# Performance work log

Measured on AMD Instinct MI355X. Metric: run time of the kernel, lower is better.

## Reference

```python
import jax, jax.numpy as jnp
import numpy as np

D_MODEL, N_HEADS, D_K, BASE, EPS = 1024, 16, 64, 10000, 1e-6
SCALE = 1.0 / np.sqrt(D_K)


def rope(x):
    # x: [b, s, h, d]
    b, s, h, d = x.shape
    d2 = d // 2
    theta = 1.0 / (BASE ** (jnp.arange(0, d, 2, dtype=jnp.float32) / d))  # [d2]
    idx_theta = jnp.arange(s, dtype=jnp.float32)[:, None] * theta[None, :]  # [s, d2]
    idx_theta2 = jnp.concatenate([idx_theta, idx_theta], axis=1)  # [s, d]
    cos = jnp.cos(idx_theta2)[None, :, None, :]
    sin = jnp.sin(idx_theta2)[None, :, None, :]
    neg_half = jnp.concatenate([-x[..., d2:], x[..., :d2]], axis=-1)
    return x * cos + neg_half * sin


def setup_inputs() -> dict:
    key = jax.random.key(0)
    ks = jax.random.split(key, 10)
    B, S = 2, 2048
    std = 1.0 / np.sqrt(D_MODEL)
    return {
        "h": jax.random.normal(ks[0], (B, S, D_MODEL), dtype=jnp.float32),
        "wq": jax.random.normal(ks[1], (D_MODEL, N_HEADS * D_K), dtype=jnp.float32) * std,
        "bq": jnp.zeros((N_HEADS * D_K,), dtype=jnp.float32),
        "wk": jax.random.normal(ks[2], (D_MODEL, N_HEADS * D_K), dtype=jnp.float32) * std,
        "bk": jnp.zeros((N_HEADS * D_K,), dtype=jnp.float32),
        "wv": jax.random.normal(ks[3], (D_MODEL, N_HEADS * D_K), dtype=jnp.float32) * std,
        "bv": jnp.zeros((N_HEADS * D_K,), dtype=jnp.float32),
        "wo": jax.random.normal(ks[4], (N_HEADS * D_K, D_MODEL), dtype=jnp.float32) * std,
        "bo": jnp.zeros((D_MODEL,), dtype=jnp.float32),
        "g": jnp.ones((D_MODEL,), dtype=jnp.float32),
    }


def reference(h, wq, bq, wk, bk, wv, bv, wo, bo, g):
    B, S, _ = h.shape
    h_res = h
    # RMSNorm
    hn = h * jax.lax.rsqrt(jnp.mean(h * h, axis=-1, keepdims=True) + EPS) * g
    mh = (B, S, N_HEADS, D_K)
    q = (hn @ wq + bq).reshape(mh)
    k = (hn @ wk + bk).reshape(mh)
    v = (hn @ wv + bv).reshape(mh)
    q, k = rope(q), rope(k)
    attn = jnp.einsum('bihd,bjhd->bhij', q, k) * SCALE
    mask = jnp.tril(jnp.ones((S, S), dtype=bool))
    attn = jnp.where(mask, attn, -jnp.inf)
    attn = jax.nn.softmax(attn, axis=-1)
    out = jnp.einsum('bhij,bjhd->bihd', attn, v).reshape(B, S, N_HEADS * D_K)
    return out @ wo + bo + h_res
```

## Files before the change

### kernel.cpp

```cpp
#include <hip/hip_runtime.h>
#include <hip/hip_bf16.h>

#define D_MODEL 1024
#define NH 16
#define DK 64
#define SEQ 2048
#define BATCH 2
#define NTOK (BATCH * SEQ)
#define EPS 1e-6f

typedef __attribute__((ext_vector_type(4))) float f32x4;
typedef __attribute__((ext_vector_type(16))) float f32x16;
typedef __attribute__((ext_vector_type(8))) short s16x8;
typedef unsigned int u32;
typedef __hip_bfloat16 bf16;

#define AS1 __attribute__((address_space(1)))
#define AS3 __attribute__((address_space(3)))

static __device__ __forceinline__ s16x8 ld8(const bf16* p) {
    return *reinterpret_cast<const s16x8*>(p);
}
static __device__ __forceinline__ float b2f(short s) {
    return __uint_as_float(((u32)(unsigned short)s) << 16);
}

static __device__ __forceinline__ u32 cvtpk(float lo, float hi) {
    u32 r;
    asm volatile("v_cvt_pk_bf16_f32 %0, %1, %2" : "=v"(r) : "v"(lo), "v"(hi));
    return r;
}
static __device__ __forceinline__ void swap32(u32& a, u32& b) {
    asm volatile("v_permlane32_swap_b32 %0, %1" : "+v"(a), "+v"(b));
}
static __device__ __forceinline__ float exp2f_fast(float x) {
    float r;
    asm("v_exp_f32 %0, %1" : "=v"(r) : "v"(x));
    return r;
}
static __device__ __forceinline__ void gld_lds16(const bf16* g, bf16* l) {
    __builtin_amdgcn_global_load_lds((const AS1 void*)g, (AS3 void*)l, 16, 0, 0);
}

union W4 { s16x8 v; u32 w[4]; };

#define LDSW(arr, row, kc) ld8(&arr[(row)][(((kc) ^ ((row) & 7)) << 3)])

__global__ __launch_bounds__(256) void k_prep(const float* __restrict__ h,
                                              const float* __restrict__ g,
                                              const float* __restrict__ wq,
                                              const float* __restrict__ wk,
                                              const float* __restrict__ wv,
                                              const float* __restrict__ wo,
                                              bf16* __restrict__ hn,
                                              bf16* __restrict__ wallT,
                                              float2* __restrict__ tab) {
    const int bid = blockIdx.x;
    const int tid = threadIdx.x;
    if (bid < 4096) {
        const int row = bid;
        const float4 x = reinterpret_cast<const float4*>(h + (size_t)row * D_MODEL)[tid];
        float ss = x.x * x.x + x.y * x.y + x.z * x.z + x.w * x.w;
#pragma unroll
        for (int off = 32; off; off >>= 1) ss += __shfl_xor(ss, off);
        __shared__ float red[4];
        if ((tid & 63) == 0) red[tid >> 6] = ss;
        __syncthreads();
        const float tot = red[0] + red[1] + red[2] + red[3];
        const float rs = rsqrtf(tot * (1.0f / D_MODEL) + EPS);
        const float4 gg = reinterpret_cast<const float4*>(g)[tid];
        bf16* o = hn + (size_t)row * D_MODEL + tid * 4;
        o[0] = __float2bfloat16(x.x * rs * gg.x);
        o[1] = __float2bfloat16(x.y * rs * gg.y);
        o[2] = __float2bfloat16(x.z * rs * gg.z);
        o[3] = __float2bfloat16(x.w * rs * gg.w);
        if (row < 256) {
            const int idx = row * 256 + tid;
            const int s = idx >> 5, i = idx & 31;
            const float theta = __expf(-(float)i * 0.28782313662425572f);
            float sn, cs;
            sincosf((float)s * theta, &sn, &cs);
            tab[idx] = make_float2(cs, sn);
        }
    } else {
        __shared__ float t[32][33];
        const int bid2 = bid - 4096;
        const int kt = (bid2 & 31) * 32;
        const int by = bid2 >> 5;
        const int nt = by * 32;
        const float* W = (by < 32) ? wq : (by < 64) ? wk : (by < 96) ? wv : wo;
        const int nl = nt & (D_MODEL - 1);
        const int tx = tid & 31, ty = tid >> 5;
#pragma unroll
        for (int i = 0; i < 4; i++)
            t[ty + 8 * i][tx] = W[(size_t)(kt + ty + 8 * i) * D_MODEL + nl + tx];
        __syncthreads();
#pragma unroll
        for (int i = 0; i < 4; i++)
            wallT[(size_t)(nt + ty + 8 * i) * D_MODEL + kt + tx] = __float2bfloat16(t[tx][ty + 8 * i]);
    }
}

__global__ __launch_bounds__(256) void k_gemm64_qkv(const bf16* __restrict__ A,
                                                    const bf16* __restrict__ Bt,
                                                    const float* __restrict__ bq,
                                                    const float* __restrict__ bk,
                                                    const float* __restrict__ bv,
                                                    const float2* __restrict__ tab,
                                                    bf16* __restrict__ qb,
                                                    bf16* __restrict__ kpk,
                                                    bf16* __restrict__ vpk) {
    __shared__ __align__(16) char smem[32768];
    const int tid = threadIdx.x;
    const int w = tid >> 6, lane = tid & 63, l16 = lane & 15, lq = lane >> 4;
    const int wr = w >> 1, wc = w & 1;
    const int col0 = blockIdx.x * 64;
    const int row0 = blockIdx.y * 64;
    const int grow = lane >> 3;
    const int scol = (((lane & 7) ^ grow) << 3);

    auto stage = [&](int buf, int t) {
        bf16* as = (bf16*)(smem + buf * 16384);
        bf16* bs = (bf16*)(smem + buf * 16384 + 8192);
        const int k0 = t << 6;
        gld_lds16(A + (size_t)(row0 + w * 16 + grow) * D_MODEL + k0 + scol,      as + (w * 16) * 64);
        gld_lds16(A + (size_t)(row0 + w * 16 + 8 + grow) * D_MODEL + k0 + scol,  as + (w * 16 + 8) * 64);
        gld_lds16(Bt + (size_t)(col0 + w * 16 + grow) * D_MODEL + k0 + scol,     bs + (w * 16) * 64);
        gld_lds16(Bt + (size_t)(col0 + w * 16 + 8 + grow) * D_MODEL + k0 + scol, bs + (w * 16 + 8) * 64);
    };

    f32x4 acc[2][2];
#pragma unroll
    for (int i = 0; i < 2; i++)
#pragma unroll
        for (int j = 0; j < 2; j++) acc[i][j] = f32x4{0, 0, 0, 0};

    stage(0, 0);
    __syncthreads();
    int buf = 0;
    for (int t = 0; t < 16; t++) {
        if (t < 15) stage(buf ^ 1, t + 1);
        bf16(*As)[64] = (bf16(*)[64])(smem + buf * 16384);
        bf16(*Bs)[64] = (bf16(*)[64])(smem + buf * 16384 + 8192);
        s16x8 af[2][2], bfr[2][2];
#pragma unroll
        for (int mi = 0; mi < 2; mi++)
#pragma unroll
            for (int ks = 0; ks < 2; ks++)
                af[mi][ks] = LDSW(As, wr * 32 + mi * 16 + l16, ks * 4 + lq);
#pragma unroll
        for (int ni = 0; ni < 2; ni++)
#pragma unroll
            for (int ks = 0; ks < 2; ks++)
                bfr[ni][ks] = LDSW(Bs, wc * 32 + ni * 16 + l16, ks * 4 + lq);
        __builtin_amdgcn_s_setprio(1);
#pragma unroll
        for (int ks = 0; ks < 2; ks++)
#pragma unroll
            for (int mi = 0; mi < 2; mi++)
#pragma unroll
                for (int ni = 0; ni < 2; ni++)
                    acc[mi][ni] = __builtin_amdgcn_mfma_f32_16x16x32_bf16(af[mi][ks], bfr[ni][ks], acc[mi][ni], 0, 0, 0);
        __builtin_amdgcn_s_setprio(0);
        __syncthreads();
        buf ^= 1;
    }

    const int sect = col0 >> 10;
    const int b_ = row0 >> 11;
    const int head = (col0 & 1023) >> 6;
    if (sect == 2) {
        const int e0 = (lq & 1) * 4;
        const int tileL = (row0 & (SEQ - 1)) >> 6;
        bf16* dstH = vpk + ((size_t)(b_ * NH + head) << 17);
#pragma unroll
        for (int ni = 0; ni < 2; ni++) {
            const int dloc = wc * 32 + ni * 16 + l16;
            const float bs = bv[(col0 & 1023) + dloc];
#pragma unroll
            for (int mi = 0; mi < 2; mi++) {
                const int m = wr * 2 + mi;
                size_t off = ((((size_t)(tileL * 2 + (dloc >> 5)) * 4 + m) * 64
                               + ((lq >> 1) & 1) * 32 + (dloc & 31)) << 3) + e0;
                uint2 pv;
                pv.x = cvtpk(acc[mi][ni][0] + bs, acc[mi][ni][1] + bs);
                pv.y = cvtpk(acc[mi][ni][2] + bs, acc[mi][ni][3] + bs);
                *reinterpret_cast<uint2*>(dstH + off) = pv;
            }
        }
        return;
    }
    bf16(*Cs)[72] = (bf16(*)[72])smem;
    const float* bias = (sect == 0) ? bq : bk;
#pragma unroll
    for (int ni = 0; ni < 2; ni++) {
        const int cl = wc * 32 + ni * 16 + l16;
        const float bs = bias[(col0 & 1023) + cl];
#pragma unroll
        for (int mi = 0; mi < 2; mi++) {
            const int rl = wr * 32 + mi * 16 + lq * 4;
#pragma unroll
            for (int r = 0; r < 4; r++)
                Cs[rl + r][cl] = __float2bfloat16(acc[mi][ni][r] + bs);
        }
    }
    __syncthreads();
    const int row = tid >> 2, q = tid & 3;
    const int s_ = (row0 + row) & (SEQ - 1);
    const float2* tb = tab + s_ * 32 + q * 8;
    const float qs = (sect == 0) ? 0.18033688011112042f : 1.0f;
    const s16x8 vlo = ld8(&Cs[row][q * 8]);
    const s16x8 vhi = ld8(&Cs[row][q * 8 + 32]);
    u32 plo[4], phi[4];
#pragma unroll
    for (int e2 = 0; e2 < 4; e2++) {
        float a[2], b[2];
#pragma unroll
        for (int k = 0; k < 2; k++) {
            const int e = e2 * 2 + k;
            const float2 cs = tb[e];
            const float x1 = b2f(vlo[e]), x2 = b2f(vhi[e]);
            a[k] = (x1 * cs.x - x2 * cs.y) * qs;
            b[k] = (x2 * cs.x + x1 * cs.y) * qs;
        }
        plo[e2] = cvtpk(a[0], a[1]);
        phi[e2] = cvtpk(b[0], b[1]);
    }
    if (sect == 0) {
        bf16* qdst = qb + (((size_t)(b_ * NH + head) * SEQ + s_) << 6);
        *reinterpret_cast<uint4*>(qdst + q * 8)      = make_uint4(plo[0], plo[1], plo[2], plo[3]);
        *reinterpret_cast<uint4*>(qdst + 32 + q * 8) = make_uint4(phi[0], phi[1], phi[2], phi[3]);
    } else {
        bf16* kdst = kpk + ((size_t)(b_ * NH + head) << 17);
        const int jb = s_ >> 5, j31 = s_ & 31;
        const size_t offL = (((size_t)(jb * 4 + (q >> 1)) * 64 + (q & 1) * 32 + j31) << 3);
        const size_t offH = (((size_t)(jb * 4 + ((q + 4) >> 1)) * 64 + ((q + 4) & 1) * 32 + j31) << 3);
        *reinterpret_cast<uint4*>(kdst + offL) = make_uint4(plo[0], plo[1], plo[2], plo[3]);
        *reinterpret_cast<uint4*>(kdst + offH) = make_uint4(phi[0], phi[1], phi[2], phi[3]);
    }
}

__global__ __launch_bounds__(256) void k_attn9(const bf16* __restrict__ qg,
                                               const bf16* __restrict__ kp,
                                               const bf16* __restrict__ vp,
                                               bf16* __restrict__ ao) {
    const int tid = threadIdx.x;
    const int w = tid >> 6;
    const int lane = tid & 63;
    const int l31 = lane & 31;
    const int hi = lane >> 5;
    const int bid = blockIdx.x;
    const int blk = (bid >> 3) & 15;
    const int bh  = (bid & 7) + ((bid >> 7) << 3);
    int pos;
    switch (w) {
        case 0:  pos = blk;      break;
        case 1:  pos = 31 - blk; break;
        case 2:  pos = 32 + blk; break;
        default: pos = 63 - blk; break;
    }
    const int qw = pos << 5;
    const int qrow = qw + l31;

    const bf16* qptr = qg + (((size_t)bh * SEQ + qrow) << 6) + 8 * hi;
    s16x8 qf[4];
#pragma unroll
    for (int t = 0; t < 4; t++) qf[t] = ld8(qptr + 16 * t);

    f32x16 o0, o1;
#pragma unroll
    for (int r = 0; r < 16; r++) { o0[r] = 0.0f; o1[r] = 0.0f; }
    float l4[4] = {0.0f, 0.0f, 0.0f, 0.0f};

    const int nfull = qw >> 6;
    const int ntot  = (qw + 95) >> 6;
    const bf16* kbase = kp + ((size_t)bh << 17);
    const bf16* vbase = vp + ((size_t)bh << 17);

    s16x8 kA[8], kB[8], vC[8];
#pragma unroll
    for (int t = 0; t < 8; t++) kA[t] = ld8(kbase + (((size_t)t * 64 + lane) << 3));

    auto att_step = [&](s16x8(&KC)[8], s16x8(&KN)[8], const int kt) {
        const int kb = kt << 6;
#pragma unroll
        for (int t = 0; t < 8; t++)
            vC[t] = ld8(vbase + (((size_t)(kt * 8 + t) * 64 + lane) << 3));
        f32x16 s0, s1;
#pragma unroll
        for (int r = 0; r < 16; r++) { s0[r] = 0.0f; s1[r] = 0.0f; }
        __builtin_amdgcn_s_setprio(1);
#pragma unroll
        for (int t = 0; t < 4; t++) {
            s0 = __builtin_amdgcn_mfma_f32_32x32x16_bf16(KC[t],     qf[t], s0, 0, 0, 0);
            s1 = __builtin_amdgcn_mfma_f32_32x32x16_bf16(KC[4 + t], qf[t], s1, 0, 0, 0);
        }
        __builtin_amdgcn_s_setprio(0);
        const int ktn = (kt + 1 < ntot) ? kt + 1 : kt;
#pragma unroll
        for (int t = 0; t < 8; t++)
            KN[t] = ld8(kbase + (((size_t)(ktn * 8 + t) * 64 + lane) << 3));
        float p[32];
#pragma unroll
        for (int r = 0; r < 16; r++) { p[r] = s0[r]; p[16 + r] = s1[r]; }
        if (kt >= nfull) {
#pragma unroll
            for (int r = 0; r < 32; r++) {
                const int j = kb + 8 * (r >> 2) + (r & 3) + 4 * hi;
                if (j > qrow) p[r] = -3.0e38f;
            }
        }
#pragma unroll
        for (int r = 0; r < 32; r++) { p[r] = exp2f_fast(p[r]); l4[r & 3] += p[r]; }
        u32 pk_[16];
#pragma unroll
        for (int a = 0; a < 8; a++) {
            pk_[2 * a]     = cvtpk(p[4 * a],     p[4 * a + 1]);
            pk_[2 * a + 1] = cvtpk(p[4 * a + 2], p[4 * a + 3]);
        }
        __builtin_amdgcn_s_setprio(1);
#pragma unroll
        for (int m = 0; m < 4; m++) {
            u32 b0 = pk_[4 * m],     b2 = pk_[4 * m + 2];
            u32 b1 = pk_[4 * m + 1], b3 = pk_[4 * m + 3];
            swap32(b0, b2);
            swap32(b1, b3);
            W4 B; B.w[0] = b0; B.w[1] = b1; B.w[2] = b2; B.w[3] = b3;
            o0 = __builtin_amdgcn_mfma_f32_32x32x16_bf16(vC[m],     B.v, o0, 0, 0, 0);
            o1 = __builtin_amdgcn_mfma_f32_32x32x16_bf16(vC[4 + m], B.v, o1, 0, 0, 0);
        }
        __builtin_amdgcn_s_setprio(0);
    };

    int kt = 0;
    for (;;) {
        att_step(kA, kB, kt); if (++kt == ntot) break;
        att_step(kB, kA, kt); if (++kt == ntot) break;
    }

    float rs = (l4[0] + l4[1]) + (l4[2] + l4[3]);
    rs += __shfl_xor(rs, 32);
    const float inv = 1.0f / rs;
    const int b_ = bh >> 4, h_ = bh & (NH - 1);
    bf16* orow = ao + (((size_t)(b_ * SEQ + qrow)) << 10) + (h_ << 6);
#pragma unroll
    for (int g = 0; g < 4; g++) {
        {
            uint2 val;
            val.x = cvtpk(o0[4 * g] * inv, o0[4 * g + 1] * inv);
            val.y = cvtpk(o0[4 * g + 2] * inv, o0[4 * g + 3] * inv);
            *reinterpret_cast<uint2*>(orow + 8 * g + 4 * hi) = val;
        }
        {
            uint2 val;
            val.x = cvtpk(o1[4 * g] * inv, o1[4 * g + 1] * inv);
            val.y = cvtpk(o1[4 * g + 2] * inv, o1[4 * g + 3] * inv);
            *reinterpret_cast<uint2*>(orow + 32 + 8 * g + 4 * hi) = val;
        }
    }
}

__global__ __launch_bounds__(256) void k_gemm64_out(const bf16* __restrict__ A,
                                                    const bf16* __restrict__ Bt,
                                                    const float* __restrict__ bo,
                                                    const float* __restrict__ hres,
                                                    float* __restrict__ out) {
    __shared__ __align__(16) char smem[32768];
    const int tid = threadIdx.x;
    const int w = tid >> 6, lane = tid & 63, l16 = lane & 15, lq = lane >> 4;
    const int wr = w >> 1, wc = w & 1;
    const int col0 = blockIdx.x * 64;
    const int row0 = blockIdx.y * 64;
    const int grow = lane >> 3;
    const int scol = (((lane & 7) ^ grow) << 3);

    auto stage = [&](int buf, int t) {
        bf16* as = (bf16*)(smem + buf * 16384);
        bf16* bs = (bf16*)(smem + buf * 16384 + 8192);
        const int k0 = t << 6;
        gld_lds16(A + (size_t)(row0 + w * 16 + grow) * D_MODEL + k0 + scol,      as + (w * 16) * 64);
        gld_lds16(A + (size_t)(row0 + w * 16 + 8 + grow) * D_MODEL + k0 + scol,  as + (w * 16 + 8) * 64);
        gld_lds16(Bt + (size_t)(col0 + w * 16 + grow) * D_MODEL + k0 + scol,     bs + (w * 16) * 64);
        gld_lds16(Bt + (size_t)(col0 + w * 16 + 8 + grow) * D_MODEL + k0 + scol, bs + (w * 16 + 8) * 64);
    };

    f32x4 acc[2][2];
#pragma unroll
    for (int i = 0; i < 2; i++)
#pragma unroll
        for (int j = 0; j < 2; j++) acc[i][j] = f32x4{0, 0, 0, 0};

    stage(0, 0);
    __syncthreads();
    int buf = 0;
    for (int t = 0; t < 16; t++) {
        if (t < 15) stage(buf ^ 1, t + 1);
        bf16(*As)[64] = (bf16(*)[64])(smem + buf * 16384);
        bf16(*Bs)[64] = (bf16(*)[64])(smem + buf * 16384 + 8192);
        s16x8 af[2][2], bfr[2][2];
#pragma unroll
        for (int mi = 0; mi < 2; mi++)
#pragma unroll
            for (int ks = 0; ks < 2; ks++)
                af[mi][ks] = LDSW(As, wr * 32 + mi * 16 + l16, ks * 4 + lq);
#pragma unroll
        for (int ni = 0; ni < 2; ni++)
#pragma unroll
            for (int ks = 0; ks < 2; ks++)
                bfr[ni][ks] = LDSW(Bs, wc * 32 + ni * 16 + l16, ks * 4 + lq);
        __builtin_amdgcn_s_setprio(1);
#pragma unroll
        for (int ks = 0; ks < 2; ks++)
#pragma unroll
            for (int mi = 0; mi < 2; mi++)
#pragma unroll
                for (int ni = 0; ni < 2; ni++)
                    acc[mi][ni] = __builtin_amdgcn_mfma_f32_16x16x32_bf16(af[mi][ks], bfr[ni][ks], acc[mi][ni], 0, 0, 0);
        __builtin_amdgcn_s_setprio(0);
        __syncthreads();
        buf ^= 1;
    }
#pragma unroll
    for (int ni = 0; ni < 2; ni++) {
        const int col = col0 + wc * 32 + ni * 16 + l16;
        const float bs = bo[col];
#pragma unroll
        for (int mi = 0; mi < 2; mi++) {
#pragma unroll
            for (int r = 0; r < 4; r++) {
                const int row = row0 + wr * 32 + mi * 16 + lq * 4 + r;
                out[(size_t)row * D_MODEL + col] =
                    acc[mi][ni][r] + bs + hres[(size_t)row * D_MODEL + col];
            }
        }
    }
}

extern "C" void kernel_launch(void* const* d_in, const int* in_sizes, int n_in,
                              void* d_out, int out_size, void* d_ws, size_t ws_size,
                              hipStream_t stream) {
    (void)in_sizes; (void)n_in; (void)out_size; (void)ws_size;
    const float* h  = (const float*)d_in[0];
    const float* wq = (const float*)d_in[1];
    const float* bq = (const float*)d_in[2];
    const float* wk = (const float*)d_in[3];
    const float* bk = (const float*)d_in[4];
    const float* wv = (const float*)d_in[5];
    const float* bv = (const float*)d_in[6];
    const float* wo = (const float*)d_in[7];
    const float* bo = (const float*)d_in[8];
    const float* g  = (const float*)d_in[9];
    float* out = (float*)d_out;

    char* ws = (char*)d_ws;
    size_t off = 0;
    auto carve = [&](size_t bytes) {
        void* p = ws + off;
        off += (bytes + 255) & ~(size_t)255;
        return p;
    };
    bf16* hn    = (bf16*)carve((size_t)NTOK * D_MODEL * 2);
    bf16* wallT = (bf16*)carve((size_t)4 * D_MODEL * D_MODEL * 2);
    bf16* wqkvT = wallT;
    bf16* woT   = wallT + (size_t)3 * D_MODEL * D_MODEL;
    bf16* qb    = (bf16*)carve((size_t)BATCH * NH * SEQ * DK * 2);
    bf16* kpk   = (bf16*)carve((size_t)BATCH * NH * SEQ * DK * 2);
    bf16* vpk   = (bf16*)carve((size_t)BATCH * NH * SEQ * DK * 2);
    bf16* ao    = (bf16*)carve((size_t)NTOK * D_MODEL * 2);
    float2* tab = (float2*)carve((size_t)SEQ * 32 * sizeof(float2));

    k_prep<<<8192, 256, 0, stream>>>(h, g, wq, wk, wv, wo, hn, wallT, tab);
    k_gemm64_qkv<<<dim3(48, 64), 256, 0, stream>>>(hn, wqkvT, bq, bk, bv, tab, qb, kpk, vpk);
    k_attn9<<<512, 256, 0, stream>>>(qb, kpk, vpk, ao);
    k_gemm64_out<<<dim3(16, 64), 256, 0, stream>>>(ao, woT, bo, h, out);
}
```

Before: 107.4 us.

## Enlarge QKV and output GEMM tiles to 128x128 with K-step 32

Measured after the change: 120.0 us. +11.7%, slower.

```diff
diff --git a/kernel.cpp b/kernel.cpp
--- a/kernel.cpp
+++ b/kernel.cpp
@@ -44,7 +44,7 @@
 
 union W4 { s16x8 v; u32 w[4]; };
 
-#define LDSW(arr, row, kc) ld8(&arr[(row)][(((kc) ^ ((row) & 7)) << 3)])
+#define SW32C(row, kc) ((((kc) ^ (((row) >> 1) & 3))) << 3)
 
 __global__ __launch_bounds__(256) void k_prep(const float* __restrict__ h,
                                               const float* __restrict__ g,
@@ -101,66 +101,64 @@
     }
 }
 
-__global__ __launch_bounds__(256) void k_gemm64_qkv(const bf16* __restrict__ A,
-                                                    const bf16* __restrict__ Bt,
-                                                    const float* __restrict__ bq,
-                                                    const float* __restrict__ bk,
-                                                    const float* __restrict__ bv,
-                                                    const float2* __restrict__ tab,
-                                                    bf16* __restrict__ qb,
-                                                    bf16* __restrict__ kpk,
-                                                    bf16* __restrict__ vpk) {
+__global__ __launch_bounds__(256) void k_gemm128_qkv(const bf16* __restrict__ A,
+                                                     const bf16* __restrict__ Bt,
+                                                     const float* __restrict__ bq,
+                                                     const float* __restrict__ bk,
+                                                     const float* __restrict__ bv,
+                                                     const float2* __restrict__ tab,
+                                                     bf16* __restrict__ qb,
+                                                     bf16* __restrict__ kpk,
+                                                     bf16* __restrict__ vpk) {
     __shared__ __align__(16) char smem[32768];
     const int tid = threadIdx.x;
     const int w = tid >> 6, lane = tid & 63, l16 = lane & 15, lq = lane >> 4;
     const int wr = w >> 1, wc = w & 1;
-    const int col0 = blockIdx.x * 64;
-    const int row0 = blockIdx.y * 64;
-    const int grow = lane >> 3;
-    const int scol = (((lane & 7) ^ grow) << 3);
+    const int col0 = blockIdx.x * 128;
+    const int row0 = blockIdx.y * 128;
+    const int grow = lane >> 2;
+    const int scol = SW32C(grow, lane & 3);
 
     auto stage = [&](int buf, int t) {
         bf16* as = (bf16*)(smem + buf * 16384);
         bf16* bs = (bf16*)(smem + buf * 16384 + 8192);
-        const int k0 = t << 6;
-        gld_lds16(A + (size_t)(row0 + w * 16 + grow) * D_MODEL + k0 + scol,      as + (w * 16) * 64);
-        gld_lds16(A + (size_t)(row0 + w * 16 + 8 + grow) * D_MODEL + k0 + scol,  as + (w * 16 + 8) * 64);
-        gld_lds16(Bt + (size_t)(col0 + w * 16 + grow) * D_MODEL + k0 + scol,     bs + (w * 16) * 64);
-        gld_lds16(Bt + (size_t)(col0 + w * 16 + 8 + grow) * D_MODEL + k0 + scol, bs + (w * 16 + 8) * 64);
+        const int k0 = t << 5;
+        gld_lds16(A + (size_t)(row0 + w * 16 + grow) * D_MODEL + k0 + scol,       as + (w * 16) * 32);
+        gld_lds16(A + (size_t)(row0 + 64 + w * 16 + grow) * D_MODEL + k0 + scol,  as + (64 + w * 16) * 32);
+        gld_lds16(Bt + (size_t)(col0 + w * 16 + grow) * D_MODEL + k0 + scol,      bs + (w * 16) * 32);
+        gld_lds16(Bt + (size_t)(col0 + 64 + w * 16 + grow) * D_MODEL + k0 + scol, bs + (64 + w * 16) * 32);
     };
 
-    f32x4 acc[2][2];
-#pragma unroll
-    for (int i = 0; i < 2; i++)
-#pragma unroll
-        for (int j = 0; j < 2; j++) acc[i][j] = f32x4{0, 0, 0, 0};
+    f32x4 acc[4][4];
+#pragma unroll
+    for (int i = 0; i < 4; i++)
+#pragma unroll
+        for (int j = 0; j < 4; j++) acc[i][j] = f32x4{0, 0, 0, 0};
 
     stage(0, 0);
     __syncthreads();
     int buf = 0;
-    for (int t = 0; t < 16; t++) {
-        if (t < 15) stage(buf ^ 1, t + 1);
-        bf16(*As)[64] = (bf16(*)[64])(smem + buf * 16384);
-        bf16(*Bs)[64] = (bf16(*)[64])(smem + buf * 16384 + 8192);
-        s16x8 af[2][2], bfr[2][2];
-#pragma unroll
-        for (int mi = 0; mi < 2; mi++)
-#pragma unroll
-            for (int ks = 0; ks < 2; ks++)
-                af[mi][ks] = LDSW(As, wr * 32 + mi * 16 + l16, ks * 4 + lq);
-#pragma unroll
-        for (int ni = 0; ni < 2; ni++)
-#pragma unroll
-            for (int ks = 0; ks < 2; ks++)
-                bfr[ni][ks] = LDSW(Bs, wc * 32 + ni * 16 + l16, ks * 4 + lq);
+    for (int t = 0; t < 32; t++) {
+        if (t < 31) stage(buf ^ 1, t + 1);
+        bf16(*As)[32] = (bf16(*)[32])(smem + buf * 16384);
+        bf16(*Bs)[32] = (bf16(*)[32])(smem + buf * 16384 + 8192);
+        s16x8 af[4], bfr[4];
+#pragma unroll
+        for (int mi = 0; mi < 4; mi++) {
+            const int rr = wr * 64 + mi * 16 + l16;
+            af[mi] = ld8(&As[rr][SW32C(rr, lq)]);
+        }
+#pragma unroll
+        for (int ni = 0; ni < 4; ni++) {
+            const int rr = wc * 64 + ni * 16 + l16;
+            bfr[ni] = ld8(&Bs[rr][SW32C(rr, lq)]);
+        }
         __builtin_amdgcn_s_setprio(1);
 #pragma unroll
-        for (int ks = 0; ks < 2; ks++)
-#pragma unroll
-            for (int mi = 0; mi < 2; mi++)
-#pragma unroll
-                for (int ni = 0; ni < 2; ni++)
-                    acc[mi][ni] = __builtin_amdgcn_mfma_f32_16x16x32_bf16(af[mi][ks], bfr[ni][ks], acc[mi][ni], 0, 0, 0);
+        for (int mi = 0; mi < 4; mi++)
+#pragma unroll
+            for (int ni = 0; ni < 4; ni++)
+                acc[mi][ni] = __builtin_amdgcn_mfma_f32_16x16x32_bf16(af[mi], bfr[ni], acc[mi][ni], 0, 0, 0);
         __builtin_amdgcn_s_setprio(0);
         __syncthreads();
         buf ^= 1;
@@ -168,20 +166,19 @@
 
     const int sect = col0 >> 10;
     const int b_ = row0 >> 11;
-    const int head = (col0 & 1023) >> 6;
     if (sect == 2) {
+        const int head = ((col0 & 1023) >> 6) + wc;
+        const int tileL = ((row0 & (SEQ - 1)) >> 6) + wr;
         const int e0 = (lq & 1) * 4;
-        const int tileL = (row0 & (SEQ - 1)) >> 6;
         bf16* dstH = vpk + ((size_t)(b_ * NH + head) << 17);
 #pragma unroll
-        for (int ni = 0; ni < 2; ni++) {
-            const int dloc = wc * 32 + ni * 16 + l16;
-            const float bs = bv[(col0 & 1023) + dloc];
-#pragma unroll
-            for (int mi = 0; mi < 2; mi++) {
-                const int m = wr * 2 + mi;
-                size_t off = ((((size_t)(tileL * 2 + (dloc >> 5)) * 4 + m) * 64
-                               + ((lq >> 1) & 1) * 32 + (dloc & 31)) << 3) + e0;
+        for (int ni = 0; ni < 4; ni++) {
+            const int dloc = ni * 16 + l16;
+            const float bs = bv[(col0 & 1023) + wc * 64 + dloc];
+#pragma unroll
+            for (int mi = 0; mi < 4; mi++) {
+                size_t off = ((((size_t)(tileL * 2 + (dloc >> 5)) * 4 + mi) * 64
+                               + (lq >> 1) * 32 + (dloc & 31)) << 3) + e0;
                 uint2 pv;
                 pv.x = cvtpk(acc[mi][ni][0] + bs, acc[mi][ni][1] + bs);
                 pv.y = cvtpk(acc[mi][ni][2] + bs, acc[mi][ni][3] + bs);
@@ -190,53 +187,60 @@
         }
         return;
     }
-    bf16(*Cs)[72] = (bf16(*)[72])smem;
     const float* bias = (sect == 0) ? bq : bk;
 #pragma unroll
-    for (int ni = 0; ni < 2; ni++) {
-        const int cl = wc * 32 + ni * 16 + l16;
+    for (int ni = 0; ni < 4; ni++) {
+        const int cl = wc * 64 + ni * 16 + l16;
         const float bs = bias[(col0 & 1023) + cl];
 #pragma unroll
-        for (int mi = 0; mi < 2; mi++) {
-            const int rl = wr * 32 + mi * 16 + lq * 4;
-#pragma unroll
-            for (int r = 0; r < 4; r++)
-                Cs[rl + r][cl] = __float2bfloat16(acc[mi][ni][r] + bs);
+        for (int mi = 0; mi < 4; mi++) {
+            const int rl = wr * 64 + mi * 16 + lq * 4;
+#pragma unroll
+            for (int r = 0; r < 4; r++) {
+                const int rr = rl + r;
+                *(bf16*)(smem + (((rr * 256) + cl * 2) ^ ((rr & 15) << 4))) =
+                    __float2bfloat16(acc[mi][ni][r] + bs);
+            }
         }
     }
     __syncthreads();
-    const int row = tid >> 2, q = tid & 3;
+    const int row = tid >> 1, ch = tid & 1;
     const int s_ = (row0 + row) & (SEQ - 1);
-    const float2* tb = tab + s_ * 32 + q * 8;
+    const int head = ((col0 & 1023) >> 6) + ch;
+    const float2* tb = tab + s_ * 32;
     const float qs = (sect == 0) ? 0.18033688011112042f : 1.0f;
-    const s16x8 vlo = ld8(&Cs[row][q * 8]);
-    const s16x8 vhi = ld8(&Cs[row][q * 8 + 32]);
-    u32 plo[4], phi[4];
-#pragma unroll
-    for (int e2 = 0; e2 < 4; e2++) {
-        float a[2], b[2];
-#pragma unroll
-        for (int k = 0; k < 2; k++) {
-            const int e = e2 * 2 + k;
-            const float2 cs = tb[e];
-            const float x1 = b2f(vlo[e]), x2 = b2f(vhi[e]);
-            a[k] = (x1 * cs.x - x2 * cs.y) * qs;
-            b[k] = (x2 * cs.x + x1 * cs.y) * qs;
-        }
-        plo[e2] = cvtpk(a[0], a[1]);
-        phi[e2] = cvtpk(b[0], b[1]);
-    }
-    if (sect == 0) {
-        bf16* qdst = qb + (((size_t)(b_ * NH + head) * SEQ + s_) << 6);
-        *reinterpret_cast<uint4*>(qdst + q * 8)      = make_uint4(plo[0], plo[1], plo[2], plo[3]);
-        *reinterpret_cast<uint4*>(qdst + 32 + q * 8) = make_uint4(phi[0], phi[1], phi[2], phi[3]);
-    } else {
-        bf16* kdst = kpk + ((size_t)(b_ * NH + head) << 17);
-        const int jb = s_ >> 5, j31 = s_ & 31;
-        const size_t offL = (((size_t)(jb * 4 + (q >> 1)) * 64 + (q & 1) * 32 + j31) << 3);
-        const size_t offH = (((size_t)(jb * 4 + ((q + 4) >> 1)) * 64 + ((q + 4) & 1) * 32 + j31) << 3);
-        *reinterpret_cast<uint4*>(kdst + offL) = make_uint4(plo[0], plo[1], plo[2], plo[3]);
-        *reinterpret_cast<uint4*>(kdst + offH) = make_uint4(phi[0], phi[1], phi[2], phi[3]);
+    bf16* qdst = qb + (((size_t)(b_ * NH + head) * SEQ + s_) << 6);
+    bf16* kdst = kpk + ((size_t)(b_ * NH + head) << 17);
+    const int jb = s_ >> 5, j31 = s_ & 31;
+#pragma unroll
+    for (int c = 0; c < 4; c++) {
+        const int clo = ch * 8 + c, chi = clo + 4;
+        const s16x8 vlo = ld8((const bf16*)(smem + row * 256 + ((clo ^ (row & 15)) << 4)));
+        const s16x8 vhi = ld8((const bf16*)(smem + row * 256 + ((chi ^ (row & 15)) << 4)));
+        u32 plo[4], phi[4];
+#pragma unroll
+        for (int e2 = 0; e2 < 4; e2++) {
+            float a[2], b[2];
+#pragma unroll
+            for (int k = 0; k < 2; k++) {
+                const int e = e2 * 2 + k;
+                const float2 cs = tb[c * 8 + e];
+                const float x1 = b2f(vlo[e]), x2 = b2f(vhi[e]);
+                a[k] = (x1 * cs.x - x2 * cs.y) * qs;
+                b[k] = (x2 * cs.x + x1 * cs.y) * qs;
+            }
+            plo[e2] = cvtpk(a[0], a[1]);
+            phi[e2] = cvtpk(b[0], b[1]);
+        }
+        if (sect == 0) {
+            *reinterpret_cast<uint4*>(qdst + c * 8)      = make_uint4(plo[0], plo[1], plo[2], plo[3]);
+            *reinterpret_cast<uint4*>(qdst + 32 + c * 8) = make_uint4(phi[0], phi[1], phi[2], phi[3]);
+        } else {
+            const size_t offL = (((size_t)(jb * 4 + (c >> 1)) * 64 + (c & 1) * 32 + j31) << 3);
+            const size_t offH = (((size_t)(jb * 4 + ((c + 4) >> 1)) * 64 + ((c + 4) & 1) * 32 + j31) << 3);
+            *reinterpret_cast<uint4*>(kdst + offL) = make_uint4(plo[0], plo[1], plo[2], plo[3]);
+            *reinterpret_cast<uint4*>(kdst + offH) = make_uint4(phi[0], phi[1], phi[2], phi[3]);
+        }
     }
 }
 
@@ -360,75 +364,73 @@
     }
 }
 
-__global__ __launch_bounds__(256) void k_gemm64_out(const bf16* __restrict__ A,
-                                                    const bf16* __restrict__ Bt,
-                                                    const float* __restrict__ bo,
-                                                    const float* __restrict__ hres,
-                                                    float* __restrict__ out) {
+__global__ __launch_bounds__(256) void k_gemm128_out(const bf16* __restrict__ A,
+                                                     const bf16* __restrict__ Bt,
+                                                     const float* __restrict__ bo,
+                                                     const float* __restrict__ hres,
+                                                     float* __restrict__ out) {
     __shared__ __align__(16) char smem[32768];
     const int tid = threadIdx.x;
     const int w = tid >> 6, lane = tid & 63, l16 = lane & 15, lq = lane >> 4;
     const int wr = w >> 1, wc = w & 1;
-    const int col0 = blockIdx.x * 64;
-    const int row0 = blockIdx.y * 64;
-    const int grow = lane >> 3;
-    const int scol = (((lane & 7) ^ grow) << 3);
+    const int col0 = blockIdx.x * 128;
+    const int row0 = blockIdx.y * 128;
+    const int grow = lane >> 2;
+    const int scol = SW32C(grow, lane & 3);
 
     auto stage = [&](int buf, int t) {
         bf16* as = (bf16*)(smem + buf * 16384);
         bf16* bs = (bf16*)(smem + buf * 16384 + 8192);
-        const int k0 = t << 6;
-        gld_lds16(A + (size_t)(row0 + w * 16 + grow) * D_MODEL + k0 + scol,      as + (w * 16) * 64);
-        gld_lds16(A + (size_t)(row0 + w * 16 + 8 + grow) * D_MODEL + k0 + scol,  as + (w * 16 + 8) * 64);
-        gld_lds16(Bt + (size_t)(col0 + w * 16 + grow) * D_MODEL + k0 + scol,     bs + (w * 16) * 64);
-        gld_lds16(Bt + (size_t)(col0 + w * 16 + 8 + grow) * D_MODEL + k0 + scol, bs + (w * 16 + 8) * 64);
+        const int k0 = t << 5;
+        gld_lds16(A + (size_t)(row0 + w * 16 + grow) * D_MODEL + k0 + scol,       as + (w * 16) * 32);
+        gld_lds16(A + (size_t)(row0 + 64 + w * 16 + grow) * D_MODEL + k0 + scol,  as + (64 + w * 16) * 32);
+        gld_lds16(Bt + (size_t)(col0 + w * 16 + grow) * D_MODEL + k0 + scol,      bs + (w * 16) * 32);
+        gld_lds16(Bt + (size_t)(col0 + 64 + w * 16 + grow) * D_MODEL + k0 + scol, bs + (64 + w * 16) * 32);
     };
 
-    f32x4 acc[2][2];
-#pragma unroll
-    for (int i = 0; i < 2; i++)
-#pragma unroll
-        for (int j = 0; j < 2; j++) acc[i][j] = f32x4{0, 0, 0, 0};
+    f32x4 acc[4][4];
+#pragma unroll
+    for (int i = 0; i < 4; i++)
+#pragma unroll
+        for (int j = 0; j < 4; j++) acc[i][j] = f32x4{0, 0, 0, 0};
 
     stage(0, 0);
     __syncthreads();
     int buf = 0;
-    for (int t = 0; t < 16; t++) {
-        if (t < 15) stage(buf ^ 1, t + 1);
-        bf16(*As)[64] = (bf16(*)[64])(smem + buf * 16384);
-        bf16(*Bs)[64] = (bf16(*)[64])(smem + buf * 16384 + 8192);
-        s16x8 af[2][2], bfr[2][2];
-#pragma unroll
-        for (int mi = 0; mi < 2; mi++)
-#pragma unroll
-            for (int ks = 0; ks < 2; ks++)
-                af[mi][ks] = LDSW(As, wr * 32 + mi * 16 + l16, ks * 4 + lq);
-#pragma unroll
-        for (int ni = 0; ni < 2; ni++)
-#pragma unroll
-            for (int ks = 0; ks < 2; ks++)
-                bfr[ni][ks] = LDSW(Bs, wc * 32 + ni * 16 + l16, ks * 4 + lq);
+    for (int t = 0; t < 32; t++) {
+        if (t < 31) stage(buf ^ 1, t + 1);
+        bf16(*As)[32] = (bf16(*)[32])(smem + buf * 16384);
+        bf16(*Bs)[32] = (bf16(*)[32])(smem + buf * 16384 + 8192);
+        s16x8 af[4], bfr[4];
+#pragma unroll
+        for (int mi = 0; mi < 4; mi++) {
+            const int rr = wr * 64 + mi * 16 + l16;
+            af[mi] = ld8(&As[rr][SW32C(rr, lq)]);
+        }
+#pragma unroll
+        for (int ni = 0; ni < 4; ni++) {
+            const int rr = wc * 64 + ni * 16 + l16;
+            bfr[ni] = ld8(&Bs[rr][SW32C(rr, lq)]);
+        }
         __builtin_amdgcn_s_setprio(1);
 #pragma unroll
-        for (int ks = 0; ks < 2; ks++)
-#pragma unroll
-            for (int mi = 0; mi < 2; mi++)
-#pragma unroll
-                for (int ni = 0; ni < 2; ni++)
-                    acc[mi][ni] = __builtin_amdgcn_mfma_f32_16x16x32_bf16(af[mi][ks], bfr[ni][ks], acc[mi][ni], 0, 0, 0);
+        for (int mi = 0; mi < 4; mi++)
+#pragma unroll
+            for (int ni = 0; ni < 4; ni++)
+                acc[mi][ni] = __builtin_amdgcn_mfma_f32_16x16x32_bf16(af[mi], bfr[ni], acc[mi][ni], 0, 0, 0);
         __builtin_amdgcn_s_setprio(0);
         __syncthreads();
         buf ^= 1;
     }
 #pragma unroll
-    for (int ni = 0; ni < 2; ni++) {
-        const int col = col0 + wc * 32 + ni * 16 + l16;
+    for (int ni = 0; ni < 4; ni++) {
+        const int col = col0 + wc * 64 + ni * 16 + l16;
         const float bs = bo[col];
 #pragma unroll
-        for (int mi = 0; mi < 2; mi++) {
+        for (int mi = 0; mi < 4; mi++) {
 #pragma unroll
             for (int r = 0; r < 4; r++) {
-                const int row = row0 + wr * 32 + mi * 16 + lq * 4 + r;
+                const int row = row0 + wr * 64 + mi * 16 + lq * 4 + r;
                 out[(size_t)row * D_MODEL + col] =
                     acc[mi][ni][r] + bs + hres[(size_t)row * D_MODEL + col];
             }
@@ -470,7 +472,7 @@
     float2* tab = (float2*)carve((size_t)SEQ * 32 * sizeof(float2));
 
     k_prep<<<8192, 256, 0, stream>>>(h, g, wq, wk, wv, wo, hn, wallT, tab);
-    k_gemm64_qkv<<<dim3(48, 64), 256, 0, stream>>>(hn, wqkvT, bq, bk, bv, tab, qb, kpk, vpk);
+    k_gemm128_qkv<<<dim3(24, 32), 256, 0, stream>>>(hn, wqkvT, bq, bk, bv, tab, qb, kpk, vpk);
     k_attn9<<<512, 256, 0, stream>>>(qb, kpk, vpk, ao);
-    k_gemm64_out<<<dim3(16, 64), 256, 0, stream>>>(ao, woT, bo, h, out);
-}
+    k_gemm128_out<<<dim3(8, 32), 256, 0, stream>>>(ao, woT, bo, h, out);
+}
```

## Triple-buffer QKV and output GEMM K-loop with one barrier per step

Applied to the files above, without the earlier changes.

Measured after the change: 112.6 us. 4.8% more time.

```diff
diff --git a/kernel.cpp b/kernel.cpp
--- a/kernel.cpp
+++ b/kernel.cpp
@@ -110,7 +110,7 @@
                                                     bf16* __restrict__ qb,
                                                     bf16* __restrict__ kpk,
                                                     bf16* __restrict__ vpk) {
-    __shared__ __align__(16) char smem[32768];
+    __shared__ __align__(16) char smem[49152];
     const int tid = threadIdx.x;
     const int w = tid >> 6, lane = tid & 63, l16 = lane & 15, lq = lane >> 4;
     const int wr = w >> 1, wc = w & 1;
@@ -119,9 +119,9 @@
     const int grow = lane >> 3;
     const int scol = (((lane & 7) ^ grow) << 3);
 
-    auto stage = [&](int buf, int t) {
-        bf16* as = (bf16*)(smem + buf * 16384);
-        bf16* bs = (bf16*)(smem + buf * 16384 + 8192);
+    auto stage = [&](int slot, int t) {
+        bf16* as = (bf16*)(smem + slot * 16384);
+        bf16* bs = (bf16*)(smem + slot * 16384 + 8192);
         const int k0 = t << 6;
         gld_lds16(A + (size_t)(row0 + w * 16 + grow) * D_MODEL + k0 + scol,      as + (w * 16) * 64);
         gld_lds16(A + (size_t)(row0 + w * 16 + 8 + grow) * D_MODEL + k0 + scol,  as + (w * 16 + 8) * 64);
@@ -136,12 +136,15 @@
         for (int j = 0; j < 2; j++) acc[i][j] = f32x4{0, 0, 0, 0};
 
     stage(0, 0);
-    __syncthreads();
-    int buf = 0;
+    stage(1, 1);
+#pragma unroll 1
     for (int t = 0; t < 16; t++) {
-        if (t < 15) stage(buf ^ 1, t + 1);
-        bf16(*As)[64] = (bf16(*)[64])(smem + buf * 16384);
-        bf16(*Bs)[64] = (bf16(*)[64])(smem + buf * 16384 + 8192);
+        if (t < 15) asm volatile("s_waitcnt vmcnt(4)" ::: "memory");
+        else        asm volatile("s_waitcnt vmcnt(0)" ::: "memory");
+        __builtin_amdgcn_s_barrier();
+        if (t + 2 < 16) stage((t + 2) % 3, t + 2);
+        bf16(*As)[64] = (bf16(*)[64])(smem + (t % 3) * 16384);
+        bf16(*Bs)[64] = (bf16(*)[64])(smem + (t % 3) * 16384 + 8192);
         s16x8 af[2][2], bfr[2][2];
 #pragma unroll
         for (int mi = 0; mi < 2; mi++)
@@ -162,8 +165,6 @@
                 for (int ni = 0; ni < 2; ni++)
                     acc[mi][ni] = __builtin_amdgcn_mfma_f32_16x16x32_bf16(af[mi][ks], bfr[ni][ks], acc[mi][ni], 0, 0, 0);
         __builtin_amdgcn_s_setprio(0);
-        __syncthreads();
-        buf ^= 1;
     }
 
     const int sect = col0 >> 10;
@@ -190,6 +191,7 @@
         }
         return;
     }
+    __syncthreads();
     bf16(*Cs)[72] = (bf16(*)[72])smem;
     const float* bias = (sect == 0) ? bq : bk;
 #pragma unroll
@@ -365,7 +367,7 @@
                                                     const float* __restrict__ bo,
                                                     const float* __restrict__ hres,
                                                     float* __restrict__ out) {
-    __shared__ __align__(16) char smem[32768];
+    __shared__ __align__(16) char smem[49152];
     const int tid = threadIdx.x;
     const int w = tid >> 6, lane = tid & 63, l16 = lane & 15, lq = lane >> 4;
     const int wr = w >> 1, wc = w & 1;
@@ -374,9 +376,9 @@
     const int grow = lane >> 3;
     const int scol = (((lane & 7) ^ grow) << 3);
 
-    auto stage = [&](int buf, int t) {
-        bf16* as = (bf16*)(smem + buf * 16384);
-        bf16* bs = (bf16*)(smem + buf * 16384 + 8192);
+    auto stage = [&](int slot, int t) {
+        bf16* as = (bf16*)(smem + slot * 16384);
+        bf16* bs = (bf16*)(smem + slot * 16384 + 8192);
         const int k0 = t << 6;
         gld_lds16(A + (size_t)(row0 + w * 16 + grow) * D_MODEL + k0 + scol,      as + (w * 16) * 64);
         gld_lds16(A + (size_t)(row0 + w * 16 + 8 + grow) * D_MODEL + k0 + scol,  as + (w * 16 + 8) * 64);
@@ -391,12 +393,15 @@
         for (int j = 0; j < 2; j++) acc[i][j] = f32x4{0, 0, 0, 0};
 
     stage(0, 0);
-    __syncthreads();
-    int buf = 0;
+    stage(1, 1);
+#pragma unroll 1
     for (int t = 0; t < 16; t++) {
-        if (t < 15) stage(buf ^ 1, t + 1);
-        bf16(*As)[64] = (bf16(*)[64])(smem + buf * 16384);
-        bf16(*Bs)[64] = (bf16(*)[64])(smem + buf * 16384 + 8192);
+        if (t < 15) asm volatile("s_waitcnt vmcnt(4)" ::: "memory");
+        else        asm volatile("s_waitcnt vmcnt(0)" ::: "memory");
+        __builtin_amdgcn_s_barrier();
+        if (t + 2 < 16) stage((t + 2) % 3, t + 2);
+        bf16(*As)[64] = (bf16(*)[64])(smem + (t % 3) * 16384);
+        bf16(*Bs)[64] = (bf16(*)[64])(smem + (t % 3) * 16384 + 8192);
         s16x8 af[2][2], bfr[2][2];
 #pragma unroll
         for (int mi = 0; mi < 2; mi++)
@@ -417,8 +422,6 @@
                 for (int ni = 0; ni < 2; ni++)
                     acc[mi][ni] = __builtin_amdgcn_mfma_f32_16x16x32_bf16(af[mi][ks], bfr[ni][ks], acc[mi][ni], 0, 0, 0);
         __builtin_amdgcn_s_setprio(0);
-        __syncthreads();
-        buf ^= 1;
     }
 #pragma unroll
     for (int ni = 0; ni < 2; ni++) {
```
